# Optimization experiments

Hardware: AMD Instinct MI355X
Metric: run time of the kernel (lower is better)

Reference implementation:

```python
import jax, jax.numpy as jnp
import numpy as np

B, S, D = 2, 1024, 2048      # batch, seq, hidden
E, F, TOP_K = 8, 1408, 2     # experts, moe intermediate, top-k


def setup_inputs() -> dict:
    key = jax.random.key(0)
    k1, k2, k3, k4, k5 = jax.random.split(key, 5)
    scale = 0.02
    return {
        "hidden_states": jax.random.normal(k1, (B, S, D), jnp.float32),
        "gate_w": jax.random.normal(k2, (E, D), jnp.float32) * scale,   # nn.Linear weight [E, D]
        "w_gate": jax.random.normal(k3, (E, D, F), jnp.float32) * scale,  # gate_proj per expert
        "w_up": jax.random.normal(k4, (E, D, F), jnp.float32) * scale,    # up_proj per expert
        "w_down": jax.random.normal(k5, (E, F, D), jnp.float32) * scale,  # down_proj per expert
    }


def reference(hidden_states, gate_w, w_gate, w_up, w_down):
    b, s, d = hidden_states.shape
    e = gate_w.shape[0]
    x = hidden_states.reshape(-1, d)                      # [T, D], T = b*s
    t = x.shape[0]

    # router: logits -> full softmax -> top-k -> renormalize (qwen_topk_softmax, normalize_topk=True)
    logits = x @ gate_w.T                                  # [T, E]
    probs = jax.nn.softmax(logits.astype(jnp.float32), axis=-1)
    top_w, sel = jax.lax.top_k(probs, TOP_K)               # [T, K]
    top_w = top_w / jnp.sum(top_w, axis=-1, keepdims=True)
    top_w = top_w.astype(logits.dtype)

    # per-token per-expert combine weight (0 for unselected experts) == weighted scatter-add
    w_te = jnp.zeros((t, e), logits.dtype).at[jnp.arange(t)[:, None], sel].add(top_w)  # [T, E]

    # expert MLPs: SiLU(x Wg) * (x Wu) -> Wd, weighted by w_te (0-weight experts contribute 0)
    g = jnp.einsum('td,edf->tef', x, w_gate)               # [T, E, F]
    u = jnp.einsum('td,edf->tef', x, w_up)                 # [T, E, F]
    h = jax.nn.silu(g) * u
    out = jnp.einsum('tef,efd->td', h * w_te[:, :, None], w_down)  # weight before down (linear, same math)
    return out.reshape(b, s, d)
```

## Files before the change

### kernel.cpp

```cpp
#include <hip/hip_runtime.h>

typedef unsigned short u16;
typedef unsigned int   u32;

#define T_TOK 2048
#define DIM   2048
#define FDIM  1408
#define NEXP  8
#define SLOTS 4224

typedef __bf16 bf16x8 __attribute__((ext_vector_type(8)));
typedef float  f32x4  __attribute__((ext_vector_type(4)));

union B16 { uint4 u; bf16x8 v; };

__device__ __forceinline__ u16 f2bf(float f) {
  union { float f; u32 u; } c; c.f = f;
  u32 u = c.u;
  u += 0x7FFFu + ((u >> 16) & 1u);
  return (u16)(u >> 16);
}
__device__ __forceinline__ float bf2f(u16 h) {
  union { u32 u; float f; } c; c.u = (u32)h << 16; return c.f;
}

__device__ __forceinline__ void gld_lds16(const void* g, void* l) {
  __builtin_amdgcn_global_load_lds(
      (const __attribute__((address_space(1))) unsigned int*)g,
      (__attribute__((address_space(3))) unsigned int*)l, 16, 0, 0);
}

__global__ __launch_bounds__(256) void cvt_transpose(
    const float* __restrict__ Wg, const float* __restrict__ Wu, const float* __restrict__ Wd,
    u16* __restrict__ WgT, u16* __restrict__ WuT, u16* __restrict__ WdT)
{
  const int z = blockIdx.z;
  const int tensor = z >> 3;
  const int e = z & 7;
  const int Kt = (tensor == 2) ? FDIM : DIM;
  const int Nt = (tensor == 2) ? DIM : FDIM;
  const float* src;
  u16* dst;
  if (tensor == 0)      { src = Wg + (size_t)e * DIM * FDIM; dst = WgT + (size_t)e * DIM * FDIM; }
  else if (tensor == 1) { src = Wu + (size_t)e * DIM * FDIM; dst = WuT + (size_t)e * DIM * FDIM; }
  else                  { src = Wd + (size_t)e * DIM * FDIM; dst = WdT + (size_t)e * DIM * FDIM; }
  const int k0 = blockIdx.y * 64, n0 = blockIdx.x * 64;
  if (k0 >= Kt || n0 >= Nt) return;

  __shared__ u16 tile[64][68];
  const int tid = threadIdx.x;
  #pragma unroll
  for (int p = 0; p < 4; ++p) {
    int k = p * 16 + (tid >> 4);
    int n = (tid & 15) * 4;
    float4 v = *(const float4*)(src + (size_t)(k0 + k) * Nt + n0 + n);
    uint2 o;
    o.x = (u32)f2bf(v.x) | ((u32)f2bf(v.y) << 16);
    o.y = (u32)f2bf(v.z) | ((u32)f2bf(v.w) << 16);
    *(uint2*)(&tile[k][n]) = o;
  }
  __syncthreads();
  #pragma unroll
  for (int p = 0; p < 2; ++p) {
    int n  = p * 32 + (tid >> 3);
    int kc = (tid & 7) * 8;
    u16 r[8];
    #pragma unroll
    for (int j = 0; j < 8; ++j) r[j] = tile[kc + j][n];
    uint4 o;
    o.x = (u32)r[0] | ((u32)r[1] << 16);
    o.y = (u32)r[2] | ((u32)r[3] << 16);
    o.z = (u32)r[4] | ((u32)r[5] << 16);
    o.w = (u32)r[6] | ((u32)r[7] << 16);
    *(uint4*)(dst + (size_t)(n0 + n) * Kt + k0 + kc) = o;
  }
}

__global__ __launch_bounds__(256) void router_kernel(
    const float* __restrict__ x, const float* __restrict__ gate_w,
    int* __restrict__ sel, float* __restrict__ wgt, int* __restrict__ counts)
{
  const int t = blockIdx.x;
  const float* xr = x + (size_t)t * DIM;
  float acc[NEXP];
  #pragma unroll
  for (int e = 0; e < NEXP; ++e) acc[e] = 0.f;
  for (int d = threadIdx.x; d < DIM; d += 256) {
    float xv = xr[d];
    #pragma unroll
    for (int e = 0; e < NEXP; ++e) acc[e] += xv * gate_w[e * DIM + d];
  }
  #pragma unroll
  for (int e = 0; e < NEXP; ++e) {
    #pragma unroll
    for (int s = 32; s > 0; s >>= 1) acc[e] += __shfl_down(acc[e], s, 64);
  }
  __shared__ float red[4][NEXP];
  const int lane = threadIdx.x & 63, wv = threadIdx.x >> 6;
  if (lane == 0) {
    #pragma unroll
    for (int e = 0; e < NEXP; ++e) red[wv][e] = acc[e];
  }
  __syncthreads();
  if (threadIdx.x == 0) {
    float l[NEXP];
    #pragma unroll
    for (int e = 0; e < NEXP; ++e) l[e] = red[0][e] + red[1][e] + red[2][e] + red[3][e];
    int i0 = 0;
    #pragma unroll
    for (int e = 1; e < NEXP; ++e) if (l[e] > l[i0]) i0 = e;
    int i1 = (i0 == 0) ? 1 : 0;
    #pragma unroll
    for (int e = 0; e < NEXP; ++e) if (e != i0 && l[e] > l[i1]) i1 = e;
    float w0 = 1.f / (1.f + __expf(l[i1] - l[i0]));
    sel[t * 2] = i0; sel[t * 2 + 1] = i1;
    wgt[t * 2] = w0; wgt[t * 2 + 1] = 1.f - w0;
    atomicAdd(&counts[i0], 1);
    atomicAdd(&counts[i1], 1);
  }
}

__global__ void scan_kernel(const int* __restrict__ counts, int* __restrict__ offs)
{
  if (threadIdx.x == 0) {
    int s = 0;
    for (int e = 0; e < NEXP; ++e) { offs[e] = s; s += counts[e]; }
    offs[NEXP] = s;
  }
}

__global__ __launch_bounds__(256) void gather_kernel(
    const float* __restrict__ x, const int* __restrict__ sel, const float* __restrict__ wgt,
    const int* __restrict__ offs, int* __restrict__ fill,
    int* __restrict__ slot_token, float* __restrict__ slot_w,
    int* __restrict__ tok_slots, u16* __restrict__ Xg)
{
  const int id = blockIdx.x;
  const int t = id >> 1;
  __shared__ int s_slot;
  if (threadIdx.x == 0) {
    int e = sel[id];
    int pos = atomicAdd(&fill[e], 1);
    int slot = offs[e] + pos;
    s_slot = slot;
    slot_token[slot] = t;
    slot_w[slot] = wgt[id];
    tok_slots[id] = slot;
  }
  __syncthreads();
  const int slot = s_slot;
  const float* src = x + (size_t)t * DIM + threadIdx.x * 8;
  float4 a = *(const float4*)(src);
  float4 b = *(const float4*)(src + 4);
  uint4 o;
  o.x = (u32)f2bf(a.x) | ((u32)f2bf(a.y) << 16);
  o.y = (u32)f2bf(a.z) | ((u32)f2bf(a.w) << 16);
  o.z = (u32)f2bf(b.x) | ((u32)f2bf(b.y) << 16);
  o.w = (u32)f2bf(b.z) | ((u32)f2bf(b.w) << 16);
  *(uint4*)(Xg + (size_t)slot * DIM + threadIdx.x * 8) = o;
}

__global__ __launch_bounds__(256, 4) void moe_gemm1(
    const u16* __restrict__ Xg,
    const u16* __restrict__ WgT, const u16* __restrict__ WuT,
    const int* __restrict__ offs, const float* __restrict__ slot_w,
    u16* __restrict__ H)
{
  const int e = blockIdx.z;
  const int off = offs[e];
  const int cnt = offs[e + 1] - off;
  const int m0 = blockIdx.y * 128;
  if (m0 >= cnt) return;
  const int n0 = blockIdx.x * 64;

  const u16* __restrict__ Bg_g = WgT + (size_t)e * (size_t)FDIM * DIM;
  const u16* __restrict__ Bu_g = WuT + (size_t)e * (size_t)FDIM * DIM;

  __shared__ __align__(16) u16 As[2][128 * 32];
  __shared__ __align__(16) u16 Bgs[2][64 * 32];
  __shared__ __align__(16) u16 Bus[2][64 * 32];

  const int tid = threadIdx.x;
  const int lane = tid & 63, wave = tid >> 6;
  const int wr = wave >> 1, wc = wave & 1;
  const int quad = lane >> 4, mr = lane & 15;
  const int qs   = (((lane & 3) ^ ((lane >> 3) & 3))) * 8;
  const int xorc = ((quad ^ ((mr >> 1) & 3))) * 8;

  const u16* agp0 = Xg + (size_t)(off + m0 + wave * 32 + (lane >> 2)) * DIM + qs;
  const u16* agp1 = agp0 + (size_t)16 * DIM;
  const u16* bgp  = Bg_g + (size_t)(n0 + wave * 16 + (lane >> 2)) * DIM + qs;
  const u16* bup  = Bu_g + (size_t)(n0 + wave * 16 + (lane >> 2)) * DIM + qs;
  const int a_lds0 = (wave * 32) * 32;
  const int a_lds1 = (wave * 32 + 16) * 32;
  const int b_lds  = (wave * 16) * 32;

  f32x4 accg[4][2], accu[4][2];
  #pragma unroll
  for (int i = 0; i < 4; ++i)
    #pragma unroll
    for (int j = 0; j < 2; ++j) { accg[i][j] = {0.f,0.f,0.f,0.f}; accu[i][j] = {0.f,0.f,0.f,0.f}; }

  gld_lds16(agp0, &As[0][a_lds0]);
  gld_lds16(agp1, &As[0][a_lds1]);
  gld_lds16(bgp,  &Bgs[0][b_lds]);
  gld_lds16(bup,  &Bus[0][b_lds]);

  int p = 0;
  for (int k0 = 0; k0 < DIM; k0 += 32, p ^= 1) {
    __syncthreads();
    if (k0 + 32 < DIM) {
      gld_lds16(agp0 + k0 + 32, &As[p ^ 1][a_lds0]);
      gld_lds16(agp1 + k0 + 32, &As[p ^ 1][a_lds1]);
      gld_lds16(bgp  + k0 + 32, &Bgs[p ^ 1][b_lds]);
      gld_lds16(bup  + k0 + 32, &Bus[p ^ 1][b_lds]);
    }
    bf16x8 af[4], bgf[2], buf2[2];
    #pragma unroll
    for (int mf = 0; mf < 4; ++mf) {
      B16 t_; t_.u = *(const uint4*)(&As[p][(wr * 64 + mf * 16 + mr) * 32 + xorc]);
      af[mf] = t_.v;
    }
    #pragma unroll
    for (int nf = 0; nf < 2; ++nf) {
      B16 tg; tg.u = *(const uint4*)(&Bgs[p][(wc * 32 + nf * 16 + mr) * 32 + xorc]);
      B16 tu; tu.u = *(const uint4*)(&Bus[p][(wc * 32 + nf * 16 + mr) * 32 + xorc]);
      bgf[nf] = tg.v; buf2[nf] = tu.v;
    }
    #pragma unroll
    for (int nf = 0; nf < 2; ++nf)
      #pragma unroll
      for (int mf = 0; mf < 4; ++mf) {
        accg[mf][nf] = __builtin_amdgcn_mfma_f32_16x16x32_bf16(af[mf], bgf[nf],  accg[mf][nf], 0, 0, 0);
        accu[mf][nf] = __builtin_amdgcn_mfma_f32_16x16x32_bf16(af[mf], buf2[nf], accu[mf][nf], 0, 0, 0);
      }
  }

  #pragma unroll
  for (int mf = 0; mf < 4; ++mf) {
    #pragma unroll
    for (int r = 0; r < 4; ++r) {
      int row = wr * 64 + mf * 16 + quad * 4 + r;
      if (m0 + row < cnt) {
        int slot = off + m0 + row;
        float w = slot_w[slot];
        #pragma unroll
        for (int nf = 0; nf < 2; ++nf) {
          float g = accg[mf][nf][r];
          float u = accu[mf][nf][r];
          float s = g / (1.f + __expf(-g));
          H[(size_t)slot * FDIM + n0 + wc * 32 + nf * 16 + mr] = f2bf(w * s * u);
        }
      }
    }
  }
}

__global__ __launch_bounds__(256, 4) void moe_gemm2(
    const u16* __restrict__ H, const u16* __restrict__ WdT,
    const int* __restrict__ offs, u16* __restrict__ Ho)
{
  const int e = blockIdx.z;
  const int off = offs[e];
  const int cnt = offs[e + 1] - off;
  const int m0 = blockIdx.y * 128;
  if (m0 >= cnt) return;
  const int n0 = blockIdx.x * 64;

  const u16* __restrict__ Bd_g = WdT + (size_t)e * (size_t)DIM * FDIM;

  __shared__ __align__(16) u16 As[2][128 * 32];
  __shared__ __align__(16) u16 Bds[2][64 * 32];

  const int tid = threadIdx.x;
  const int lane = tid & 63, wave = tid >> 6;
  const int wr = wave >> 1, wc = wave & 1;
  const int quad = lane >> 4, mr = lane & 15;
  const int qs   = (((lane & 3) ^ ((lane >> 3) & 3))) * 8;
  const int xorc = ((quad ^ ((mr >> 1) & 3))) * 8;

  const u16* agp0 = H + (size_t)(off + m0 + wave * 32 + (lane >> 2)) * FDIM + qs;
  const u16* agp1 = agp0 + (size_t)16 * FDIM;
  const u16* bdp  = Bd_g + (size_t)(n0 + wave * 16 + (lane >> 2)) * FDIM + qs;
  const int a_lds0 = (wave * 32) * 32;
  const int a_lds1 = (wave * 32 + 16) * 32;
  const int b_lds  = (wave * 16) * 32;

  f32x4 acc[4][2];
  #pragma unroll
  for (int i = 0; i < 4; ++i)
    #pragma unroll
    for (int j = 0; j < 2; ++j) acc[i][j] = {0.f,0.f,0.f,0.f};

  gld_lds16(agp0, &As[0][a_lds0]);
  gld_lds16(agp1, &As[0][a_lds1]);
  gld_lds16(bdp,  &Bds[0][b_lds]);

  int p = 0;
  for (int k0 = 0; k0 < FDIM; k0 += 32, p ^= 1) {
    __syncthreads();
    if (k0 + 32 < FDIM) {
      gld_lds16(agp0 + k0 + 32, &As[p ^ 1][a_lds0]);
      gld_lds16(agp1 + k0 + 32, &As[p ^ 1][a_lds1]);
      gld_lds16(bdp  + k0 + 32, &Bds[p ^ 1][b_lds]);
    }
    bf16x8 af[4], bdf[2];
    #pragma unroll
    for (int mf = 0; mf < 4; ++mf) {
      B16 t_; t_.u = *(const uint4*)(&As[p][(wr * 64 + mf * 16 + mr) * 32 + xorc]);
      af[mf] = t_.v;
    }
    #pragma unroll
    for (int nf = 0; nf < 2; ++nf) {
      B16 tb; tb.u = *(const uint4*)(&Bds[p][(wc * 32 + nf * 16 + mr) * 32 + xorc]);
      bdf[nf] = tb.v;
    }
    #pragma unroll
    for (int nf = 0; nf < 2; ++nf)
      #pragma unroll
      for (int mf = 0; mf < 4; ++mf)
        acc[mf][nf] = __builtin_amdgcn_mfma_f32_16x16x32_bf16(af[mf], bdf[nf], acc[mf][nf], 0, 0, 0);
  }

  #pragma unroll
  for (int mf = 0; mf < 4; ++mf) {
    #pragma unroll
    for (int r = 0; r < 4; ++r) {
      int row = wr * 64 + mf * 16 + quad * 4 + r;
      if (m0 + row < cnt) {
        int slot = off + m0 + row;
        #pragma unroll
        for (int nf = 0; nf < 2; ++nf)
          Ho[(size_t)slot * DIM + n0 + wc * 32 + nf * 16 + mr] = f2bf(acc[mf][nf][r]);
      }
    }
  }
}

__global__ __launch_bounds__(256) void combine_kernel(
    const u16* __restrict__ Ho, const int* __restrict__ tok_slots,
    float* __restrict__ out)
{
  const int t = blockIdx.x;
  const int s0 = tok_slots[t * 2], s1 = tok_slots[t * 2 + 1];
  const int base = threadIdx.x * 8;
  uint4 a = *(const uint4*)(Ho + (size_t)s0 * DIM + base);
  uint4 b = *(const uint4*)(Ho + (size_t)s1 * DIM + base);
  float* o = out + (size_t)t * DIM + base;
  float4 lo, hi;
  lo.x = bf2f((u16)(a.x & 0xFFFF)) + bf2f((u16)(b.x & 0xFFFF));
  lo.y = bf2f((u16)(a.x >> 16))    + bf2f((u16)(b.x >> 16));
  lo.z = bf2f((u16)(a.y & 0xFFFF)) + bf2f((u16)(b.y & 0xFFFF));
  lo.w = bf2f((u16)(a.y >> 16))    + bf2f((u16)(b.y >> 16));
  hi.x = bf2f((u16)(a.z & 0xFFFF)) + bf2f((u16)(b.z & 0xFFFF));
  hi.y = bf2f((u16)(a.z >> 16))    + bf2f((u16)(b.z >> 16));
  hi.z = bf2f((u16)(a.w & 0xFFFF)) + bf2f((u16)(b.w & 0xFFFF));
  hi.w = bf2f((u16)(a.w >> 16))    + bf2f((u16)(b.w >> 16));
  *(float4*)(o)     = lo;
  *(float4*)(o + 4) = hi;
}

extern "C" void kernel_launch(void* const* d_in, const int* in_sizes, int n_in,
                              void* d_out, int out_size, void* d_ws, size_t ws_size,
                              hipStream_t stream) {
  const float* x      = (const float*)d_in[0];
  const float* gate_w = (const float*)d_in[1];
  const float* w_gate = (const float*)d_in[2];
  const float* w_up   = (const float*)d_in[3];
  const float* w_down = (const float*)d_in[4];
  float* out = (float*)d_out;

  char* w = (char*)d_ws;
  int*   counts     = (int*)(w + 0);
  int*   fill       = (int*)(w + 64);
  int*   offs       = (int*)(w + 128);
  int*   sel        = (int*)(w + 4096);
  float* wgt        = (float*)(w + 4096 + 16384);
  int*   tok_slots  = (int*)(w + 4096 + 2 * 16384);
  int*   slot_token = (int*)(w + 4096 + 3 * 16384);
  float* slot_w     = (float*)(w + 4096 + 3 * 16384 + 17408);
  size_t o = 131072;
  u16* Xg  = (u16*)(w + o); o += (size_t)SLOTS * DIM  * 2;
  u16* H   = (u16*)(w + o); o += (size_t)SLOTS * FDIM * 2;
  u16* Ho  = (u16*)(w + o); o += (size_t)SLOTS * DIM  * 2;
  u16* WgT = (u16*)(w + o); o += (size_t)NEXP * DIM * FDIM * 2;
  u16* WuT = (u16*)(w + o); o += (size_t)NEXP * DIM * FDIM * 2;
  u16* WdT = (u16*)(w + o); o += (size_t)NEXP * DIM * FDIM * 2;

  hipMemsetAsync(d_ws, 0, 256, stream);

  dim3 gc(32, 32, 24);
  cvt_transpose<<<gc, 256, 0, stream>>>(w_gate, w_up, w_down, WgT, WuT, WdT);

  router_kernel<<<T_TOK, 256, 0, stream>>>(x, gate_w, sel, wgt, counts);
  scan_kernel<<<1, 64, 0, stream>>>(counts, offs);
  gather_kernel<<<T_TOK * 2, 256, 0, stream>>>(x, sel, wgt, offs, fill,
                                               slot_token, slot_w, tok_slots, Xg);

  dim3 g1(FDIM / 64, 16, NEXP);
  moe_gemm1<<<g1, 256, 0, stream>>>(Xg, WgT, WuT, offs, slot_w, H);

  dim3 g2(DIM / 64, 16, NEXP);
  moe_gemm2<<<g2, 256, 0, stream>>>(H, WdT, offs, Ho);

  combine_kernel<<<T_TOK, 256, 0, stream>>>(Ho, tok_slots, out);
}
```

Before: 575.5 us.

## Remap MoE GEMM grids per XCD and use single-buffered K=64 LDS tiles

Both expert GEMMs now use a flattened 1D grid whose block index is decoded so that blocks sharing an N-tile (the same weight columns) land on the same XCD, which should improve L2 reuse of expert weights. The K step doubles from 32 to 64 with an 8-way XOR swizzle, and the LDS double-buffering is replaced by a single buffer with a sync before and after the compute. This halves the number of barriers per K but removes the prefetch overlap between global loads and MFMA work, so load latency may become exposed.

Measured after the change: 563.2 us. -2.1%, faster.

```diff
diff --git a/kernel.cpp b/kernel.cpp
--- a/kernel.cpp
+++ b/kernel.cpp
@@ -166,74 +166,80 @@
     const int* __restrict__ offs, const float* __restrict__ slot_w,
     u16* __restrict__ H)
 {
-  const int e = blockIdx.z;
+  const int id  = blockIdx.x;
+  const int xcd = id & 7;
+  const int j   = id >> 3;
+  const int mt  = j & 15;
+  const int j2  = j >> 4;
+  const int e   = j2 & 7;
+  const int ni  = j2 >> 3;
+  const int nt  = xcd + 8 * ni;
+  if (nt >= FDIM / 64) return;
+
   const int off = offs[e];
   const int cnt = offs[e + 1] - off;
-  const int m0 = blockIdx.y * 128;
+  const int m0 = mt * 128;
   if (m0 >= cnt) return;
-  const int n0 = blockIdx.x * 64;
+  const int n0 = nt * 64;
 
   const u16* __restrict__ Bg_g = WgT + (size_t)e * (size_t)FDIM * DIM;
   const u16* __restrict__ Bu_g = WuT + (size_t)e * (size_t)FDIM * DIM;
 
-  __shared__ __align__(16) u16 As[2][128 * 32];
-  __shared__ __align__(16) u16 Bgs[2][64 * 32];
-  __shared__ __align__(16) u16 Bus[2][64 * 32];
+  __shared__ __align__(16) u16 As[128 * 64];
+  __shared__ __align__(16) u16 Bgs[64 * 64];
+  __shared__ __align__(16) u16 Bus[64 * 64];
 
   const int tid = threadIdx.x;
   const int lane = tid & 63, wave = tid >> 6;
   const int wr = wave >> 1, wc = wave & 1;
   const int quad = lane >> 4, mr = lane & 15;
-  const int qs   = (((lane & 3) ^ ((lane >> 3) & 3))) * 8;
-  const int xorc = ((quad ^ ((mr >> 1) & 3))) * 8;
-
-  const u16* agp0 = Xg + (size_t)(off + m0 + wave * 32 + (lane >> 2)) * DIM + qs;
-  const u16* agp1 = agp0 + (size_t)16 * DIM;
-  const u16* bgp  = Bg_g + (size_t)(n0 + wave * 16 + (lane >> 2)) * DIM + qs;
-  const u16* bup  = Bu_g + (size_t)(n0 + wave * 16 + (lane >> 2)) * DIM + qs;
-  const int a_lds0 = (wave * 32) * 32;
-  const int a_lds1 = (wave * 32 + 16) * 32;
-  const int b_lds  = (wave * 16) * 32;
+  const int r8 = lane >> 3;
+  const int cs = ((lane & 7) ^ (r8 & 7)) * 8;
+
+  const u16* a_base  = Xg   + (size_t)(off + m0 + wave * 32 + r8) * DIM + cs;
+  const u16* bg_base = Bg_g + (size_t)(n0 + wave * 16 + r8) * DIM + cs;
+  const u16* bu_base = Bu_g + (size_t)(n0 + wave * 16 + r8) * DIM + cs;
 
   f32x4 accg[4][2], accu[4][2];
   #pragma unroll
   for (int i = 0; i < 4; ++i)
     #pragma unroll
-    for (int j = 0; j < 2; ++j) { accg[i][j] = {0.f,0.f,0.f,0.f}; accu[i][j] = {0.f,0.f,0.f,0.f}; }
-
-  gld_lds16(agp0, &As[0][a_lds0]);
-  gld_lds16(agp1, &As[0][a_lds1]);
-  gld_lds16(bgp,  &Bgs[0][b_lds]);
-  gld_lds16(bup,  &Bus[0][b_lds]);
-
-  int p = 0;
-  for (int k0 = 0; k0 < DIM; k0 += 32, p ^= 1) {
+    for (int jj = 0; jj < 2; ++jj) { accg[i][jj] = {0.f,0.f,0.f,0.f}; accu[i][jj] = {0.f,0.f,0.f,0.f}; }
+
+  for (int k0 = 0; k0 < DIM; k0 += 64) {
+    #pragma unroll
+    for (int g = 0; g < 4; ++g)
+      gld_lds16(a_base + (size_t)g * 8 * DIM + k0, &As[(wave * 32 + g * 8) * 64]);
+    #pragma unroll
+    for (int g = 0; g < 2; ++g) {
+      gld_lds16(bg_base + (size_t)g * 8 * DIM + k0, &Bgs[(wave * 16 + g * 8) * 64]);
+      gld_lds16(bu_base + (size_t)g * 8 * DIM + k0, &Bus[(wave * 16 + g * 8) * 64]);
+    }
     __syncthreads();
-    if (k0 + 32 < DIM) {
-      gld_lds16(agp0 + k0 + 32, &As[p ^ 1][a_lds0]);
-      gld_lds16(agp1 + k0 + 32, &As[p ^ 1][a_lds1]);
-      gld_lds16(bgp  + k0 + 32, &Bgs[p ^ 1][b_lds]);
-      gld_lds16(bup  + k0 + 32, &Bus[p ^ 1][b_lds]);
+    #pragma unroll
+    for (int s = 0; s < 2; ++s) {
+      const int ca = ((4 * s + quad) ^ (mr & 7)) * 8;
+      bf16x8 af[4], bgf[2], buf2[2];
+      #pragma unroll
+      for (int mf = 0; mf < 4; ++mf) {
+        B16 t_; t_.u = *(const uint4*)(&As[(wr * 64 + mf * 16 + mr) * 64 + ca]);
+        af[mf] = t_.v;
+      }
+      #pragma unroll
+      for (int nf = 0; nf < 2; ++nf) {
+        B16 tg; tg.u = *(const uint4*)(&Bgs[(wc * 32 + nf * 16 + mr) * 64 + ca]);
+        B16 tu; tu.u = *(const uint4*)(&Bus[(wc * 32 + nf * 16 + mr) * 64 + ca]);
+        bgf[nf] = tg.v; buf2[nf] = tu.v;
+      }
+      #pragma unroll
+      for (int nf = 0; nf < 2; ++nf)
+        #pragma unroll
+        for (int mf = 0; mf < 4; ++mf) {
+          accg[mf][nf] = __builtin_amdgcn_mfma_f32_16x16x32_bf16(af[mf], bgf[nf],  accg[mf][nf], 0, 0, 0);
+          accu[mf][nf] = __builtin_amdgcn_mfma_f32_16x16x32_bf16(af[mf], buf2[nf], accu[mf][nf], 0, 0, 0);
+        }
     }
-    bf16x8 af[4], bgf[2], buf2[2];
-    #pragma unroll
-    for (int mf = 0; mf < 4; ++mf) {
-      B16 t_; t_.u = *(const uint4*)(&As[p][(wr * 64 + mf * 16 + mr) * 32 + xorc]);
-      af[mf] = t_.v;
-    }
-    #pragma unroll
-    for (int nf = 0; nf < 2; ++nf) {
-      B16 tg; tg.u = *(const uint4*)(&Bgs[p][(wc * 32 + nf * 16 + mr) * 32 + xorc]);
-      B16 tu; tu.u = *(const uint4*)(&Bus[p][(wc * 32 + nf * 16 + mr) * 32 + xorc]);
-      bgf[nf] = tg.v; buf2[nf] = tu.v;
-    }
-    #pragma unroll
-    for (int nf = 0; nf < 2; ++nf)
-      #pragma unroll
-      for (int mf = 0; mf < 4; ++mf) {
-        accg[mf][nf] = __builtin_amdgcn_mfma_f32_16x16x32_bf16(af[mf], bgf[nf],  accg[mf][nf], 0, 0, 0);
-        accu[mf][nf] = __builtin_amdgcn_mfma_f32_16x16x32_bf16(af[mf], buf2[nf], accu[mf][nf], 0, 0, 0);
-      }
+    __syncthreads();
   }
 
   #pragma unroll
@@ -260,66 +266,71 @@
     const u16* __restrict__ H, const u16* __restrict__ WdT,
     const int* __restrict__ offs, u16* __restrict__ Ho)
 {
-  const int e = blockIdx.z;
+  const int id  = blockIdx.x;
+  const int xcd = id & 7;
+  const int j   = id >> 3;
+  const int mt  = j & 15;
+  const int j2  = j >> 4;
+  const int e   = j2 & 7;
+  const int ni  = j2 >> 3;
+  const int nt  = xcd + 8 * ni;
+
   const int off = offs[e];
   const int cnt = offs[e + 1] - off;
-  const int m0 = blockIdx.y * 128;
+  const int m0 = mt * 128;
   if (m0 >= cnt) return;
-  const int n0 = blockIdx.x * 64;
+  const int n0 = nt * 64;
 
   const u16* __restrict__ Bd_g = WdT + (size_t)e * (size_t)DIM * FDIM;
 
-  __shared__ __align__(16) u16 As[2][128 * 32];
-  __shared__ __align__(16) u16 Bds[2][64 * 32];
+  __shared__ __align__(16) u16 As[128 * 64];
+  __shared__ __align__(16) u16 Bds[64 * 64];
 
   const int tid = threadIdx.x;
   const int lane = tid & 63, wave = tid >> 6;
   const int wr = wave >> 1, wc = wave & 1;
   const int quad = lane >> 4, mr = lane & 15;
-  const int qs   = (((lane & 3) ^ ((lane >> 3) & 3))) * 8;
-  const int xorc = ((quad ^ ((mr >> 1) & 3))) * 8;
-
-  const u16* agp0 = H + (size_t)(off + m0 + wave * 32 + (lane >> 2)) * FDIM + qs;
-  const u16* agp1 = agp0 + (size_t)16 * FDIM;
-  const u16* bdp  = Bd_g + (size_t)(n0 + wave * 16 + (lane >> 2)) * FDIM + qs;
-  const int a_lds0 = (wave * 32) * 32;
-  const int a_lds1 = (wave * 32 + 16) * 32;
-  const int b_lds  = (wave * 16) * 32;
+  const int r8 = lane >> 3;
+  const int cs = ((lane & 7) ^ (r8 & 7)) * 8;
+
+  const u16* a_base  = H    + (size_t)(off + m0 + wave * 32 + r8) * FDIM + cs;
+  const u16* bd_base = Bd_g + (size_t)(n0 + wave * 16 + r8) * FDIM + cs;
 
   f32x4 acc[4][2];
   #pragma unroll
   for (int i = 0; i < 4; ++i)
     #pragma unroll
-    for (int j = 0; j < 2; ++j) acc[i][j] = {0.f,0.f,0.f,0.f};
-
-  gld_lds16(agp0, &As[0][a_lds0]);
-  gld_lds16(agp1, &As[0][a_lds1]);
-  gld_lds16(bdp,  &Bds[0][b_lds]);
-
-  int p = 0;
-  for (int k0 = 0; k0 < FDIM; k0 += 32, p ^= 1) {
+    for (int jj = 0; jj < 2; ++jj) acc[i][jj] = {0.f,0.f,0.f,0.f};
+
+  for (int k0 = 0; k0 < FDIM; k0 += 64) {
+    #pragma unroll
+    for (int g = 0; g < 4; ++g)
+      gld_lds16(a_base + (size_t)g * 8 * FDIM + k0, &As[(wave * 32 + g * 8) * 64]);
+    #pragma unroll
+    for (int g = 0; g < 2; ++g)
+      gld_lds16(bd_base + (size_t)g * 8 * FDIM + k0, &Bds[(wave * 16 + g * 8) * 64]);
     __syncthreads();
-    if (k0 + 32 < FDIM) {
-      gld_lds16(agp0 + k0 + 32, &As[p ^ 1][a_lds0]);
-      gld_lds16(agp1 + k0 + 32, &As[p ^ 1][a_lds1]);
-      gld_lds16(bdp  + k0 + 32, &Bds[p ^ 1][b_lds]);
+    #pragma unroll
+    for (int s = 0; s < 2; ++s) {
+      const int ca = ((4 * s + quad) ^ (mr & 7)) * 8;
+      bf16x8 af[4], bdf[2];
+      #pragma unroll
+      for (int mf = 0; mf < 4; ++mf) {
+        B16 t_; t_.u = *(const uint4*)(&As[(wr * 64 + mf * 16 + mr) * 64 + ca]);
+        af[mf] = t_.v;
+      }
+      #pragma unroll
+      for (int nf = 0; nf < 2; ++nf) {
+        B16 tb; tb.u = *(const uint4*)(&Bds[(wc * 32 + nf * 16 + mr) * 64 + ca]);
+        bdf[nf] = tb.v;
+      }
+      #pragma unroll
+      for (int nf = 0; nf < 2; ++nf)
+        #pragma unroll
+        for (int mf = 0; mf < 4; ++mf)
+          acc[mf][nf] = __builtin_amdgcn_mfma_f32_16x16x32_bf16(af[mf], bdf[nf], acc[mf][nf], 0, 0, 0);
     }
-    bf16x8 af[4], bdf[2];
-    #pragma unroll
-    for (int mf = 0; mf < 4; ++mf) {
-      B16 t_; t_.u = *(const uint4*)(&As[p][(wr * 64 + mf * 16 + mr) * 32 + xorc]);
-      af[mf] = t_.v;
-    }
-    #pragma unroll
-    for (int nf = 0; nf < 2; ++nf) {
-      B16 tb; tb.u = *(const uint4*)(&Bds[p][(wc * 32 + nf * 16 + mr) * 32 + xorc]);
-      bdf[nf] = tb.v;
-    }
-    #pragma unroll
-    for (int nf = 0; nf < 2; ++nf)
-      #pragma unroll
-      for (int mf = 0; mf < 4; ++mf)
-        acc[mf][nf] = __builtin_amdgcn_mfma_f32_16x16x32_bf16(af[mf], bdf[nf], acc[mf][nf], 0, 0, 0);
+    __syncthreads();
   }
 
   #pragma unroll
@@ -397,11 +408,8 @@
   gather_kernel<<<T_TOK * 2, 256, 0, stream>>>(x, sel, wgt, offs, fill,
                                                slot_token, slot_w, tok_slots, Xg);
 
-  dim3 g1(FDIM / 64, 16, NEXP);
-  moe_gemm1<<<g1, 256, 0, stream>>>(Xg, WgT, WuT, offs, slot_w, H);
-
-  dim3 g2(DIM / 64, 16, NEXP);
-  moe_gemm2<<<g2, 256, 0, stream>>>(H, WdT, offs, Ho);
+  moe_gemm1<<<8 * 16 * 8 * 3, 256, 0, stream>>>(Xg, WgT, WuT, offs, slot_w, H);
+  moe_gemm2<<<8 * 16 * 8 * 4, 256, 0, stream>>>(H, WdT, offs, Ho);
 
   combine_kernel<<<T_TOK, 256, 0, stream>>>(Ho, tok_slots, out);
 }
```
